# Optimization experiments

Measured on AMD Instinct MI355X. Metric: run time of the kernel, lower is better.

Reference implementation:

```python
import jax, jax.numpy as jnp
import numpy as np

N, E, IN, H, OUT = 50000, 1600000, 128, 128, 16


def setup_inputs() -> dict:
    key = jax.random.key(0)
    ks = jax.random.split(key, 8)
    return {
        "x": jax.random.normal(ks[0], (N, IN), dtype=jnp.float32),
        "edge_index": jax.random.randint(ks[1], (2, E), 0, N, dtype=jnp.int64),
        "W1": jax.random.normal(ks[2], (IN, H), dtype=jnp.float32) * 0.05,
        "b1": jax.random.normal(ks[3], (H,), dtype=jnp.float32) * 0.05,
        "W2": jax.random.normal(ks[4], (H, H), dtype=jnp.float32) * 0.05,
        "b2": jax.random.normal(ks[5], (H,), dtype=jnp.float32) * 0.05,
        "Wc": jax.random.normal(ks[6], (H, OUT), dtype=jnp.float32) * 0.05,
        "bc": jax.random.normal(ks[7], (OUT,), dtype=jnp.float32) * 0.05,
    }


def _gcn_conv(x, src, dst, norm, W, b, n):
    # PyG GCNConv: h = x @ W; out[i] = sum_{(j->i)} norm_e * h[j]; out += b
    h = x @ W
    msg = h[src] * norm[:, None]          # [E+N, H] gather + scale
    out = jax.ops.segment_sum(msg, dst, num_segments=n)  # scatter-add
    return out + b


def reference(x, edge_index, W1, b1, W2, b2, Wc, bc):
    n = x.shape[0]
    loop = jnp.arange(n, dtype=edge_index.dtype)
    src = jnp.concatenate([edge_index[0], loop])  # add self-loops
    dst = jnp.concatenate([edge_index[1], loop])
    # symmetric normalization: deg over destinations (incl. self-loops)
    deg = jnp.zeros((n,), dtype=x.dtype).at[dst].add(1.0)
    d_inv_sqrt = jnp.where(deg > 0, jax.lax.rsqrt(deg), 0.0)
    norm = d_inv_sqrt[src] * d_inv_sqrt[dst]
    h = jax.nn.relu(_gcn_conv(x, src, dst, norm, W1, b1, n))
    # dropout p=0.5 is identity in eval mode
    h = jax.nn.relu(_gcn_conv(h, src, dst, norm, W2, b2, n))
    return h @ Wc + bc
```

## Files before the change

### kernel.cpp

```cpp
#include <hip/hip_runtime.h>
#include <hip/hip_bf16.h>


typedef unsigned int uint;
typedef unsigned short ushort;
typedef __attribute__((ext_vector_type(8))) short bf16x8;
typedef __attribute__((ext_vector_type(4))) float f32x4;

#define NPB 256
#define CAP 12288

static __device__ __forceinline__ ushort f2bf(float f) {
    unsigned u = __float_as_uint(f);
    u += 0x7fffu + ((u >> 16) & 1u);
    return (ushort)(u >> 16);
}
static __device__ __forceinline__ uint pack2(float a, float b) {
    return (uint)f2bf(a) | ((uint)f2bf(b) << 16);
}
static __device__ __forceinline__ float lo2f(uint u) { return __uint_as_float(u << 16); }
static __device__ __forceinline__ float hi2f(uint u) { return __uint_as_float(u & 0xffff0000u); }

#define UNPACK8(dst, u)                                        \
    dst[0] = lo2f(u.x); dst[1] = hi2f(u.x);                    \
    dst[2] = lo2f(u.y); dst[3] = hi2f(u.y);                    \
    dst[4] = lo2f(u.z); dst[5] = hi2f(u.z);                    \
    dst[6] = lo2f(u.w); dst[7] = hi2f(u.w);

__global__ __launch_bounds__(256) void setup(int* __restrict__ bcursor,
                                             int* __restrict__ deg,
                                             const float* __restrict__ W1,
                                             const float* __restrict__ W2,
                                             ushort* __restrict__ Wt1,
                                             ushort* __restrict__ Wt2,
                                             int n, int nbuckets) {
    int gid = blockIdx.x * 256 + threadIdx.x;
    if (gid < nbuckets) bcursor[gid] = gid * CAP;
    for (int i = gid; i < n; i += 64 * 256) deg[i] = 0;
    {
        int k = gid >> 7, nn = gid & 127;
        Wt1[nn * 128 + k] = f2bf(W1[gid]);
        Wt2[nn * 128 + k] = f2bf(W2[gid]);
    }
}

__global__ __launch_bounds__(1024) void bin_edges(const int* __restrict__ src,
                                                  const int* __restrict__ dst,
                                                  int* __restrict__ bcursor,
                                                  int* __restrict__ deg,
                                                  uint* __restrict__ pay,
                                                  int E, int nbuckets) {
    __shared__ int h[256];
    __shared__ int base[256];
    int tid = threadIdx.x;
    if (tid < 256) h[tid] = 0;
    __syncthreads();
    int chunk = (E + gridDim.x - 1) / gridDim.x;
    int i0 = blockIdx.x * chunk;
    int i1 = min(E, i0 + chunk);
    for (int i = i0 + tid; i < i1; i += 1024) {
        int d = dst[i];
        atomicAdd(&h[d >> 8], 1);
        atomicAdd(&deg[d], 1);
    }
    __syncthreads();
    if (tid < nbuckets) base[tid] = h[tid] ? atomicAdd(&bcursor[tid], h[tid]) : 0;
    __syncthreads();
    if (tid < 256) h[tid] = 0;
    __syncthreads();
    for (int i = i0 + tid; i < i1; i += 1024) {
        int d = dst[i];
        int b = d >> 8;
        int pos = base[b] + atomicAdd(&h[b], 1);
        pay[pos] = (uint)src[i] | ((uint)(d & 255) << 24);
    }
}

__global__ __launch_bounds__(512) void build_gemm1(const uint* __restrict__ pay,
                                                   const int* __restrict__ bcursor,
                                                   int* __restrict__ rowstart,
                                                   int* __restrict__ rowend,
                                                   float* __restrict__ dinv,
                                                   int* __restrict__ colidx,
                                                   const float* __restrict__ x,
                                                   const ushort* __restrict__ Wt1,
                                                   const int* __restrict__ deg,
                                                   uint* __restrict__ bufA,
                                                   int n, int nbuckets, int ntile) {
    __shared__ int s_hist[256];
    __shared__ int s_sc[256];
    __shared__ int s_cur[256];
    __shared__ __align__(16) ushort sOut[8][16][136];
    int tid = threadIdx.x;

    if ((int)blockIdx.x < nbuckets) {
        int b = blockIdx.x;
        int node0 = b * NPB;
        int s = b * CAP, e = bcursor[b];
        if (tid < 256) s_hist[tid] = 0;
        __syncthreads();
        for (int i = s + tid; i < e; i += 512) atomicAdd(&s_hist[pay[i] >> 24], 1);
        __syncthreads();
        int v = (tid < 256) ? s_hist[tid] : 0;
        if (tid < 256) s_sc[tid] = v;
        __syncthreads();
        for (int d = 1; d < 256; d <<= 1) {
            int xx = (tid < 256 && tid >= d) ? s_sc[tid - d] : 0;
            __syncthreads();
            if (tid < 256) s_sc[tid] += xx;
            __syncthreads();
        }
        if (tid < 256) {
            int excl = s_sc[tid] - v;
            s_cur[tid] = s + excl;
            int node = node0 + tid;
            if (node < n) {
                rowstart[node] = s + excl;
                rowend[node] = s + excl + v;
                dinv[node] = rsqrtf((float)(v + 1));
            }
        }
        __syncthreads();
        for (int i = s + tid; i < e; i += 512) {
            uint pp = pay[i];
            int pos = atomicAdd(&s_cur[pp >> 24], 1);
            colidx[pos] = (int)(pp & 0xffffffu);
        }
    } else {
        const int wave = tid >> 6;
        const int lane = tid & 63;
        const int quad = lane >> 4, l16 = lane & 15;
        const int tile = ((int)blockIdx.x - nbuckets) * 2 + (wave >> 2);
        const int m0 = tile * 64 + (wave & 3) * 16;
        bool active = tile < ntile;

        if (active) {
            f32x4 acc[8];
#pragma unroll
            for (int i = 0; i < 8; ++i) acc[i] = (f32x4){0.f, 0.f, 0.f, 0.f};

            int arow = m0 + l16;
            arow = arow < n ? arow : n - 1;

#pragma unroll
            for (int ks = 0; ks < 4; ++ks) {
                const float* px = &x[(size_t)arow * 128 + ks * 32 + quad * 8];
                float4 x0 = *(const float4*)px;
                float4 x1 = *(const float4*)(px + 4);
                ushort av[8] = {f2bf(x0.x), f2bf(x0.y), f2bf(x0.z), f2bf(x0.w),
                                f2bf(x1.x), f2bf(x1.y), f2bf(x1.z), f2bf(x1.w)};
                bf16x8 a = *(const bf16x8*)av;
#pragma unroll
                for (int nt = 0; nt < 8; ++nt) {
                    bf16x8 b = *(const bf16x8*)&Wt1[(size_t)(nt * 16 + l16) * 128 + ks * 32 + quad * 8];
                    acc[nt] = __builtin_amdgcn_mfma_f32_16x16x32_bf16(a, b, acc[nt], 0, 0, 0);
                }
            }

            float dv[4];
#pragma unroll
            for (int r = 0; r < 4; ++r) {
                int rr = m0 + quad * 4 + r;
                dv[r] = rsqrtf((float)(deg[rr < n ? rr : n - 1] + 1));
            }
#pragma unroll
            for (int nt = 0; nt < 8; ++nt)
#pragma unroll
                for (int r = 0; r < 4; ++r)
                    sOut[wave][quad * 4 + r][nt * 16 + l16] = f2bf(acc[nt][r] * dv[r]);
        }
        __syncthreads();

        if (active) {
#pragma unroll
            for (int i = 0; i < 4; ++i) {
                int linear = i * 64 + lane;
                int row = linear >> 4, chunk = linear & 15;
                int rr = m0 + row;
                if (rr < n) {
                    uint4 v = *(const uint4*)&sOut[wave][row][chunk * 8];
                    *(uint4*)&bufA[(size_t)rr * 64 + chunk * 4] = v;
                }
            }
        }
    }
}

static __device__ __forceinline__ void gather_q(const uint4* __restrict__ H4,
                                                int s, int e, int nn, int sub,
                                                const int* __restrict__ colidx,
                                                float acc[8]) {
    uint4 su = H4[(size_t)nn * 16 + sub];
    float t[8];
    UNPACK8(t, su);
#pragma unroll
    for (int j = 0; j < 8; ++j) acc[j] = t[j];

    int p = s;
    for (; p + 8 <= e; p += 8) {
        int c[8];
#pragma unroll
        for (int i = 0; i < 8; ++i) c[i] = colidx[p + i];
        uint4 u[8];
#pragma unroll
        for (int i = 0; i < 8; ++i) u[i] = H4[(size_t)c[i] * 16 + sub];
#pragma unroll
        for (int i = 0; i < 8; ++i) {
            float a[8];
            UNPACK8(a, u[i]);
#pragma unroll
            for (int j = 0; j < 8; ++j) acc[j] += a[j];
        }
    }
    if (p < e) {
        int c[8];
#pragma unroll
        for (int i = 0; i < 8; ++i) c[i] = (p + i < e) ? colidx[p + i] : nn;
        uint4 u[8];
#pragma unroll
        for (int i = 0; i < 8; ++i) u[i] = H4[(size_t)c[i] * 16 + sub];
#pragma unroll
        for (int i = 0; i < 8; ++i) {
            float a[8];
            UNPACK8(a, u[i]);
#pragma unroll
            for (int j = 0; j < 8; ++j) acc[j] += a[j];
        }
        float pad = (float)(p + 8 - e);
#pragma unroll
        for (int j = 0; j < 8; ++j) acc[j] -= pad * t[j];
    }
}

__global__ __launch_bounds__(256) void agg_gemm2(const uint4* __restrict__ H4,
                                                 const int* __restrict__ rowstart,
                                                 const int* __restrict__ rowend,
                                                 const int* __restrict__ colidx,
                                                 const float* __restrict__ dinv,
                                                 const float* __restrict__ b1,
                                                 const ushort* __restrict__ Wt2,
                                                 uint* __restrict__ Yb, int n) {
    __shared__ __align__(16) ushort sA[16][136];
    __shared__ __align__(16) ushort sO[16][136];
    int tid = threadIdx.x;
    int sub = tid & 15;
    int nl = tid >> 4;
    int node0 = blockIdx.x * 16;
    int node = node0 + nl;
    int nn = node < n ? node : n - 1;
    int s = rowstart[nn], e = rowend[nn];
    float di = dinv[nn];

    float acc[8];
    gather_q(H4, s, e, nn, sub, colidx, acc);
    {
        float4 c0 = ((const float4*)b1)[sub * 2];
        float4 c1 = ((const float4*)b1)[sub * 2 + 1];
        float f0 = fmaxf(fmaf(acc[0], di, c0.x), 0.f);
        float f1 = fmaxf(fmaf(acc[1], di, c0.y), 0.f);
        float f2 = fmaxf(fmaf(acc[2], di, c0.z), 0.f);
        float f3 = fmaxf(fmaf(acc[3], di, c0.w), 0.f);
        float f4 = fmaxf(fmaf(acc[4], di, c1.x), 0.f);
        float f5 = fmaxf(fmaf(acc[5], di, c1.y), 0.f);
        float f6 = fmaxf(fmaf(acc[6], di, c1.z), 0.f);
        float f7 = fmaxf(fmaf(acc[7], di, c1.w), 0.f);
        uint4 v;
        v.x = pack2(f0, f1); v.y = pack2(f2, f3);
        v.z = pack2(f4, f5); v.w = pack2(f6, f7);
        *(uint4*)&sA[nl][sub * 8] = v;
    }
    __syncthreads();

    const int wave = tid >> 6;
    const int lane = tid & 63;
    const int quad = lane >> 4, l16 = lane & 15;
    f32x4 acc2[2];
    acc2[0] = (f32x4){0.f, 0.f, 0.f, 0.f};
    acc2[1] = (f32x4){0.f, 0.f, 0.f, 0.f};
#pragma unroll
    for (int ks = 0; ks < 4; ++ks) {
        bf16x8 a = *(const bf16x8*)&sA[l16][ks * 32 + quad * 8];
#pragma unroll
        for (int t = 0; t < 2; ++t) {
            int nt = wave * 2 + t;
            bf16x8 b = *(const bf16x8*)&Wt2[(size_t)(nt * 16 + l16) * 128 + ks * 32 + quad * 8];
            acc2[t] = __builtin_amdgcn_mfma_f32_16x16x32_bf16(a, b, acc2[t], 0, 0, 0);
        }
    }
#pragma unroll
    for (int r = 0; r < 4; ++r) {
        int rr = node0 + quad * 4 + r;
        float dv = dinv[rr < n ? rr : n - 1];
#pragma unroll
        for (int t = 0; t < 2; ++t)
            sO[quad * 4 + r][(wave * 2 + t) * 16 + l16] = f2bf(acc2[t][r] * dv);
    }
    __syncthreads();

    {
        int row = tid >> 4, chunk = tid & 15;
        int rr = node0 + row;
        if (rr < n) {
            uint4 v = *(const uint4*)&sO[row][chunk * 8];
            *(uint4*)&Yb[(size_t)rr * 64 + chunk * 4] = v;
        }
    }
}

__global__ __launch_bounds__(256) void agg_out_q(const uint4* __restrict__ H4,
                                                 const int* __restrict__ rowstart,
                                                 const int* __restrict__ rowend,
                                                 const int* __restrict__ colidx,
                                                 const float* __restrict__ dinv,
                                                 const float* __restrict__ bias,
                                                 const float* __restrict__ Wc,
                                                 const float* __restrict__ bc,
                                                 float* __restrict__ out, int n) {
    __shared__ float sA[16][129];
    int tid = threadIdx.x;
    int sub = tid & 15;
    int nl = tid >> 4;
    int node = blockIdx.x * 16 + nl;
    int nn = node < n ? node : n - 1;
    int s = rowstart[nn], e = rowend[nn];
    float di = dinv[nn];

    float acc[8];
    gather_q(H4, s, e, nn, sub, colidx, acc);

    {
        float4 b0 = ((const float4*)bias)[sub * 2];
        float4 b1v = ((const float4*)bias)[sub * 2 + 1];
        float f[8];
        f[0] = fmaxf(fmaf(acc[0], di, b0.x), 0.f);
        f[1] = fmaxf(fmaf(acc[1], di, b0.y), 0.f);
        f[2] = fmaxf(fmaf(acc[2], di, b0.z), 0.f);
        f[3] = fmaxf(fmaf(acc[3], di, b0.w), 0.f);
        f[4] = fmaxf(fmaf(acc[4], di, b1v.x), 0.f);
        f[5] = fmaxf(fmaf(acc[5], di, b1v.y), 0.f);
        f[6] = fmaxf(fmaf(acc[6], di, b1v.z), 0.f);
        f[7] = fmaxf(fmaf(acc[7], di, b1v.w), 0.f);
#pragma unroll
        for (int j = 0; j < 8; ++j) sA[nl][sub * 8 + j] = f[j];
    }
    __syncthreads();

    int col = tid & 15;
    float p0 = 0.f, p1 = 0.f;
#pragma unroll 4
    for (int k = 0; k < 128; k += 2) {
        p0 = fmaf(sA[nl][k], Wc[k * 16 + col], p0);
        p1 = fmaf(sA[nl][k + 1], Wc[(k + 1) * 16 + col], p1);
    }
    if (node < n) out[(size_t)node * 16 + col] = p0 + p1 + bc[col];
}


extern "C" void kernel_launch(void* const* d_in, const int* in_sizes, int n_in,
                              void* d_out, int out_size, void* d_ws, size_t ws_size,
                              hipStream_t stream) {
    const float* x  = (const float*)d_in[0];
    const int*   ei = (const int*)d_in[1];
    const float* W1 = (const float*)d_in[2];
    const float* b1 = (const float*)d_in[3];
    const float* W2 = (const float*)d_in[4];
    const float* b2 = (const float*)d_in[5];
    const float* Wc = (const float*)d_in[6];
    const float* bc = (const float*)d_in[7];
    float* out = (float*)d_out;

    const int n = in_sizes[0] / 128;
    const int E = in_sizes[1] / 2;
    const int* src = ei;
    const int* dst = ei + E;
    const int nbuckets = (n + NPB - 1) / NPB;

    char* p = (char*)d_ws;
    auto alloc = [&](size_t bytes) {
        char* q = p;
        p += (bytes + 255) & ~(size_t)255;
        return q;
    };
    int*    bcursor  = (int*)alloc(256 * 4);
    int*    deg      = (int*)alloc((size_t)n * 4);
    int*    rowstart = (int*)alloc((size_t)n * 4);
    int*    rowend   = (int*)alloc((size_t)n * 4);
    float*  dinv     = (float*)alloc((size_t)n * 4);
    ushort* Wt1      = (ushort*)alloc(128 * 128 * 2);
    ushort* Wt2      = (ushort*)alloc(128 * 128 * 2);
    uint*   pay      = (uint*)alloc((size_t)nbuckets * CAP * 4);
    int*    colidx   = (int*)alloc((size_t)nbuckets * CAP * 4);
    uint*   bufA     = (uint*)alloc((size_t)n * 64 * 4);
    uint*   bufB     = (uint*)alloc((size_t)n * 64 * 4);
    if ((size_t)(p - (char*)d_ws) > ws_size) return;

    const int ntile = (n + 63) / 64;
    const int gblocks = (ntile + 1) / 2;
    const int aggb = (n + 15) / 16;

    setup<<<64, 256, 0, stream>>>(bcursor, deg, W1, W2, Wt1, Wt2, n, nbuckets);
    bin_edges<<<512, 1024, 0, stream>>>(src, dst, bcursor, deg, pay, E, nbuckets);
    build_gemm1<<<nbuckets + gblocks, 512, 0, stream>>>(pay, bcursor, rowstart, rowend,
                                                        dinv, colidx, x, Wt1, deg, bufA,
                                                        n, nbuckets, ntile);
    agg_gemm2<<<aggb, 256, 0, stream>>>((const uint4*)bufA, rowstart, rowend, colidx,
                                        dinv, b1, Wt2, bufB, n);
    agg_out_q<<<aggb, 256, 0, stream>>>((const uint4*)bufB, rowstart, rowend, colidx,
                                        dinv, b2, Wc, bc, out, n);
}
```

Baseline: 305.5 us.

## Split edge binning into two-pass radix partition: coarse 8 buckets then 32 sub-buckets

Edge bucketing now runs in two passes. The first pass partitions edges into 8 coarse super-buckets of 8192 destinations each, storing (src,dst) pairs. A second kernel then scatters each super-bucket into 32 fine 256-node buckets using the original packed payload. The aim is to improve write locality and cut the number of global cursor atomics compared with scattering directly into 196 buckets. In exchange it adds an extra kernel launch and an extra 8-byte-per-edge read/write pass through memory.

```diff
diff --git a/kernel.cpp b/kernel.cpp
--- a/kernel.cpp
+++ b/kernel.cpp
@@ -9,6 +9,8 @@
 
 #define NPB 256
 #define CAP 12288
+#define SCAP 278528
+#define SBLK 73
 
 static __device__ __forceinline__ ushort f2bf(float f) {
     unsigned u = __float_as_uint(f);
@@ -28,14 +30,16 @@
     dst[6] = lo2f(u.w); dst[7] = hi2f(u.w);
 
 __global__ __launch_bounds__(256) void setup(int* __restrict__ bcursor,
+                                             int* __restrict__ bcursor8,
                                              int* __restrict__ deg,
                                              const float* __restrict__ W1,
                                              const float* __restrict__ W2,
                                              ushort* __restrict__ Wt1,
                                              ushort* __restrict__ Wt2,
-                                             int n, int nbuckets) {
+                                             int n, int nbuckets, int nsb) {
     int gid = blockIdx.x * 256 + threadIdx.x;
     if (gid < nbuckets) bcursor[gid] = gid * CAP;
+    if (gid < nsb) bcursor8[gid] = gid * SCAP;
     for (int i = gid; i < n; i += 64 * 256) deg[i] = 0;
     {
         int k = gid >> 7, nn = gid & 127;
@@ -44,35 +48,71 @@
     }
 }
 
-__global__ __launch_bounds__(1024) void bin_edges(const int* __restrict__ src,
-                                                  const int* __restrict__ dst,
-                                                  int* __restrict__ bcursor,
-                                                  int* __restrict__ deg,
-                                                  uint* __restrict__ pay,
-                                                  int E, int nbuckets) {
-    __shared__ int h[256];
-    __shared__ int base[256];
+__global__ __launch_bounds__(1024) void bin8(const int* __restrict__ src,
+                                             const int* __restrict__ dst,
+                                             int* __restrict__ bcursor8,
+                                             int* __restrict__ deg,
+                                             uint2* __restrict__ pay8,
+                                             int E) {
+    __shared__ int cnt[8];
+    __shared__ int base[8];
     int tid = threadIdx.x;
-    if (tid < 256) h[tid] = 0;
+    if (tid < 8) cnt[tid] = 0;
     __syncthreads();
     int chunk = (E + gridDim.x - 1) / gridDim.x;
     int i0 = blockIdx.x * chunk;
     int i1 = min(E, i0 + chunk);
     for (int i = i0 + tid; i < i1; i += 1024) {
         int d = dst[i];
-        atomicAdd(&h[d >> 8], 1);
+        atomicAdd(&cnt[d >> 13], 1);
         atomicAdd(&deg[d], 1);
     }
     __syncthreads();
-    if (tid < nbuckets) base[tid] = h[tid] ? atomicAdd(&bcursor[tid], h[tid]) : 0;
-    __syncthreads();
-    if (tid < 256) h[tid] = 0;
+    if (tid < 8) base[tid] = cnt[tid] ? atomicAdd(&bcursor8[tid], cnt[tid]) : 0;
+    __syncthreads();
+    if (tid < 8) cnt[tid] = 0;
     __syncthreads();
     for (int i = i0 + tid; i < i1; i += 1024) {
         int d = dst[i];
-        int b = d >> 8;
-        int pos = base[b] + atomicAdd(&h[b], 1);
-        pay[pos] = (uint)src[i] | ((uint)(d & 255) << 24);
+        int b = d >> 13;
+        int pos = base[b] + atomicAdd(&cnt[b], 1);
+        pay8[pos] = make_uint2((uint)src[i], (uint)d);
+    }
+}
+
+__global__ __launch_bounds__(512) void subsort(const uint2* __restrict__ pay8,
+                                               const int* __restrict__ bcursor8,
+                                               int* __restrict__ bcursor,
+                                               uint* __restrict__ pay, int nsb) {
+    __shared__ int cnt[32];
+    __shared__ int base[32];
+    int tid = threadIdx.x;
+    int sb = blockIdx.x / SBLK;
+    int blk = blockIdx.x % SBLK;
+    if (sb >= nsb) return;
+    int s0 = sb * SCAP;
+    int e0 = bcursor8[sb];
+    int csb = e0 - s0;
+    int chunk = (csb + SBLK - 1) / SBLK;
+    int i0 = s0 + blk * chunk;
+    int i1 = min(e0, i0 + chunk);
+    if (tid < 32) cnt[tid] = 0;
+    __syncthreads();
+    for (int i = i0 + tid; i < i1; i += 512)
+        atomicAdd(&cnt[(pay8[i].y >> 8) & 31], 1);
+    __syncthreads();
+    if (tid < 32) {
+        int gb = sb * 32 + tid;
+        base[tid] = cnt[tid] ? atomicAdd(&bcursor[gb], cnt[tid]) : 0;
+    }
+    __syncthreads();
+    if (tid < 32) cnt[tid] = 0;
+    __syncthreads();
+    for (int i = i0 + tid; i < i1; i += 512) {
+        uint2 p = pay8[i];
+        int lb = (p.y >> 8) & 31;
+        int pos = base[lb] + atomicAdd(&cnt[lb], 1);
+        pay[pos] = p.x | ((p.y & 255u) << 24);
     }
 }
 
@@ -374,6 +414,7 @@
     const int* src = ei;
     const int* dst = ei + E;
     const int nbuckets = (n + NPB - 1) / NPB;
+    const int nsb = (n + 8191) / 8192;
 
     char* p = (char*)d_ws;
     auto alloc = [&](size_t bytes) {
@@ -382,12 +423,14 @@
         return q;
     };
     int*    bcursor  = (int*)alloc(256 * 4);
+    int*    bcursor8 = (int*)alloc(64 * 4);
     int*    deg      = (int*)alloc((size_t)n * 4);
     int*    rowstart = (int*)alloc((size_t)n * 4);
     int*    rowend   = (int*)alloc((size_t)n * 4);
     float*  dinv     = (float*)alloc((size_t)n * 4);
     ushort* Wt1      = (ushort*)alloc(128 * 128 * 2);
     ushort* Wt2      = (ushort*)alloc(128 * 128 * 2);
+    uint2*  pay8     = (uint2*)alloc((size_t)nsb * SCAP * 8);
     uint*   pay      = (uint*)alloc((size_t)nbuckets * CAP * 4);
     int*    colidx   = (int*)alloc((size_t)nbuckets * CAP * 4);
     uint*   bufA     = (uint*)alloc((size_t)n * 64 * 4);
@@ -398,8 +441,10 @@
     const int gblocks = (ntile + 1) / 2;
     const int aggb = (n + 15) / 16;
 
-    setup<<<64, 256, 0, stream>>>(bcursor, deg, W1, W2, Wt1, Wt2, n, nbuckets);
-    bin_edges<<<512, 1024, 0, stream>>>(src, dst, bcursor, deg, pay, E, nbuckets);
+    setup<<<64, 256, 0, stream>>>(bcursor, bcursor8, deg, W1, W2, Wt1, Wt2,
+                                  n, nbuckets, nsb);
+    bin8<<<512, 1024, 0, stream>>>(src, dst, bcursor8, deg, pay8, E);
+    subsort<<<nsb * SBLK, 512, 0, stream>>>(pay8, bcursor8, bcursor, pay, nsb);
     build_gemm1<<<nbuckets + gblocks, 512, 0, stream>>>(pay, bcursor, rowstart, rowend,
                                                         dinv, colidx, x, Wt1, deg, bufA,
                                                         n, nbuckets, ntile);
```

New measurement: 310.8 us. No clear change (+1.8%).
